# Kernel optimization log

Hardware: AMD Instinct MI355X
Metric: run time of the kernel (lower is better)

The kernel has to match this reference:

```python
import jax, jax.numpy as jnp
import numpy as np

EPS = 1e-6
STRIDES = (8, 16, 32)
IOU_THR = 0.5
GAMMA = 2.0
ALPHA = 1.0


def _ciou(b1, b2):
    # b1, b2: [..., 4] xywh boxes (broadcastable). Returns CIOU [...].
    b1xy, b1wh = b1[..., :2], b1[..., 2:]
    b2xy, b2wh = b2[..., :2], b2[..., 2:]
    b1lt, b1rb = b1xy - b1wh * 0.5, b1xy + b1wh * 0.5
    b2lt, b2rb = b2xy - b2wh * 0.5, b2xy + b2wh * 0.5
    lo1, hi1 = jnp.minimum(b1lt, b1rb), jnp.maximum(b1lt, b1rb)
    lo2, hi2 = jnp.minimum(b2lt, b2rb), jnp.maximum(b2lt, b2rb)
    area1 = (hi1[..., 0] - lo1[..., 0]) * (hi1[..., 1] - lo1[..., 1])
    area2 = (hi2[..., 0] - lo2[..., 0]) * (hi2[..., 1] - lo2[..., 1])
    iwh = jnp.clip(jnp.minimum(hi1, hi2) - jnp.maximum(lo1, lo2), 0.0, None)
    inter = iwh[..., 0] * iwh[..., 1]
    union = area1 + area2 - inter
    ious = inter / jnp.maximum(union, EPS)
    # smallest enclosing box diagonal
    owh = jnp.maximum(hi1, hi2) - jnp.minimum(lo1, lo2)
    c2 = jnp.maximum(owh[..., 0] ** 2 + owh[..., 1] ** 2, EPS)
    rho2 = jnp.sum((b1xy - b2xy) ** 2, axis=-1)
    u = rho2 / c2
    v = (4.0 / (np.pi ** 2)) * (
        jnp.arctan(b2wh[..., 0] / jnp.maximum(b2wh[..., 1], EPS))
        - jnp.arctan(b1wh[..., 0] / jnp.maximum(b1wh[..., 1], EPS))
    ) ** 2
    alpha = v / jnp.maximum(1.0 - ious + v, EPS)
    return ious - (u + alpha * v)


def _bce_logits(x, t):
    # stable BCEWithLogits, reduction='none'
    return jnp.logaddexp(0.0, x) - x * t


def _focal(x, t):
    return _bce_logits(x, t) * ALPHA * jnp.abs(t - jax.nn.sigmoid(x)) ** GAMMA


def _layer_loss(p, p_d, label, bboxes, stride):
    bs, grid = p.shape[0], p.shape[1]
    img_size = float(stride * grid)
    p_conf = p[..., 4:5]
    p_cls = p[..., 5:]
    p_d_xywh = p_d[..., :4]
    label_xywh = label[..., :4]
    obj = label[..., 4:5]
    mix = label[..., 5:6]
    label_cls = label[..., 6:]

    ciou = _ciou(p_d_xywh, label_xywh)[..., None]
    scale = 2.0 - label_xywh[..., 2:3] * label_xywh[..., 3:4] / (img_size ** 2)
    loss_ciou = obj * scale * (1.0 - ciou) * mix

    # pairwise CIOU between every pred box and up to 150 GT boxes: [bs,g,g,A,150]
    iou = _ciou(p_d_xywh[..., None, :], bboxes[:, None, None, None, :, :])
    iou_max = jnp.max(iou, axis=-1, keepdims=True)
    noobj = (1.0 - obj) * (iou_max < IOU_THR).astype(p.dtype)

    focal = _focal(p_conf, obj)
    loss_conf = (obj * focal + noobj * focal) * mix
    loss_cls = obj * _bce_logits(p_cls, label_cls) * mix

    l_ciou = jnp.sum(loss_ciou) / bs
    l_conf = jnp.sum(loss_conf) / bs
    l_cls = jnp.sum(loss_cls) / bs
    return l_ciou, l_conf, l_cls


def setup_inputs() -> dict:
    key = jax.random.key(0)
    B, A, NC, IMG = 4, 3, 20, 608
    grids = [76, 38, 19]
    inp = {}
    for i, g in enumerate(grids):
        k = jax.random.fold_in(key, i)
        ks = jax.random.split(k, 10)
        inp[f"p{i}"] = jax.random.normal(ks[0], (B, g, g, A, 5 + NC), jnp.float32)
        # decoded predictions: positive xywh in image coords + raw conf/cls
        xy = jax.random.uniform(ks[1], (B, g, g, A, 2)) * IMG
        wh = jax.random.uniform(ks[2], (B, g, g, A, 2)) * 120.0 + 2.0
        cc = jax.random.normal(ks[3], (B, g, g, A, 1 + NC))
        inp[f"p_d{i}"] = jnp.concatenate([xy, wh, cc], -1)
        # labels: xywh, obj (binary), mix (1.0), cls (binary)
        lxy = jax.random.uniform(ks[4], (B, g, g, A, 2)) * IMG
        lwh = jax.random.uniform(ks[5], (B, g, g, A, 2)) * 120.0 + 2.0
        obj = (jax.random.uniform(ks[6], (B, g, g, A, 1)) < 0.05).astype(jnp.float32)
        mix = jnp.ones((B, g, g, A, 1), jnp.float32)
        cls = (jax.random.uniform(ks[7], (B, g, g, A, NC)) < 0.5).astype(jnp.float32)
        inp[f"label{i}"] = jnp.concatenate([lxy, lwh, obj, mix, cls], -1)
        bxy = jax.random.uniform(ks[8], (B, 150, 2)) * IMG
        bwh = jax.random.uniform(ks[9], (B, 150, 2)) * 120.0 + 2.0
        inp[f"bboxes{i}"] = jnp.concatenate([bxy, bwh], -1)
    return inp


def reference(p0, p1, p2, p_d0, p_d1, p_d2, label0, label1, label2,
              bboxes0, bboxes1, bboxes2):
    ls_c, ls_conf, ls_cls = _layer_loss(p0, p_d0, label0, bboxes0, STRIDES[0])
    lm_c, lm_conf, lm_cls = _layer_loss(p1, p_d1, label1, bboxes1, STRIDES[1])
    ll_c, ll_conf, ll_cls = _layer_loss(p2, p_d2, label2, bboxes2, STRIDES[2])
    loss_ciou = ls_c + lm_c + ll_c
    loss_conf = ls_conf + lm_conf + ll_conf
    loss_cls = ls_cls + lm_cls + ll_cls
    loss = loss_ciou + loss_conf + loss_cls
    return (loss, loss_ciou, loss_conf, loss_cls)
```

## Files before the change

### kernel.cpp

```cpp
#include <hip/hip_runtime.h>
#include <math.h>

#define EPS   1e-6f
#define K_V   0.4052847345693511f
#define IMG2  369664.0f
#define NBOX  150
#define NBOXP 152
#define NCLS  20

#define BPB_L0 271
#define BPB_L1 68
#define BPB_L2 17
#define NBLK   (4*(BPB_L0+BPB_L1+BPB_L2))

#define NDW_P  1600
#define NDW_LB 1664

__device__ __forceinline__ float fast_rcp(float x) { return __builtin_amdgcn_rcpf(x); }

__device__ __forceinline__ float bce_logits(float x, float t) {
    float e = __expf(-fabsf(x));
    return fmaxf(x, 0.f) + __logf(1.f + e) - x * t;
}

__device__ __forceinline__ float wave_sum(float v) {
#pragma unroll
    for (int off = 32; off > 0; off >>= 1) v += __shfl_down(v, off, 64);
    return v;
}

__device__ __forceinline__ void stage(const float* __restrict__ g, float* s,
                                      size_t g0, size_t tot, int ndw,
                                      int wave, int lane) {
    for (int base = wave * 64; base < ndw; base += 256) {
        if (g0 + base + 64 <= tot) {
            __builtin_amdgcn_global_load_lds(
                (const __attribute__((address_space(1))) void*)(g + base + lane),
                (__attribute__((address_space(3))) void*)(s + base), 4, 0, 0);
        } else {
            int idx = base + lane;
            s[idx] = (g0 + idx < tot) ? g[idx] : 0.f;
        }
    }
}

__global__ __launch_bounds__(256, 6) void yolo_loss_kernel(
    const float* __restrict__ p0,  const float* __restrict__ pd0,
    const float* __restrict__ lb0, const float* __restrict__ bb0,
    const float* __restrict__ p1,  const float* __restrict__ pd1,
    const float* __restrict__ lb1, const float* __restrict__ bb1,
    const float* __restrict__ p2,  const float* __restrict__ pd2,
    const float* __restrict__ lb2, const float* __restrict__ bb2,
    float* __restrict__ ws, float* __restrict__ out)
{
    __shared__ float  s_pd[NDW_P], s_lb[NDW_LB], s_p[NDW_P];
    __shared__ float4 s_box[NBOXP];
    __shared__ float4 s_aux[NBOXP];
    __shared__ float  s_part[4][3];

    const int blk = blockIdx.x;
    const float *p, *pd, *lb, *bb;
    int batch, lblk, apb;
    if (blk < 4*BPB_L0) {
        p = p0; pd = pd0; lb = lb0; bb = bb0;
        batch = blk / BPB_L0; lblk = blk % BPB_L0; apb = 17328;
    } else if (blk < 4*(BPB_L0+BPB_L1)) {
        int r = blk - 4*BPB_L0;
        p = p1; pd = pd1; lb = lb1; bb = bb1;
        batch = r / BPB_L1; lblk = r % BPB_L1; apb = 4332;
    } else {
        int r = blk - 4*(BPB_L0+BPB_L1);
        p = p2; pd = pd2; lb = lb2; bb = bb2;
        batch = r / BPB_L2; lblk = r % BPB_L2; apb = 1083;
    }

    const int tid  = threadIdx.x;
    const int wave = tid >> 6, lane = tid & 63;
    const int navail = min(64, apb - lblk * 64);
    const size_t base0 = (size_t)batch * apb + (size_t)lblk * 64;

    const size_t g0p  = base0 * 25, g0lb = base0 * 26;
    const size_t totp = (size_t)apb * 100;
    const size_t totlb = (size_t)apb * 104;
    stage(pd + g0p,  s_pd, g0p,  totp,  NDW_P,  wave, lane);
    stage(lb + g0lb, s_lb, g0lb, totlb, NDW_LB, wave, lane);
    stage(p + g0p,   s_p,  g0p,  totp,  NDW_P,  wave, lane);

    if (tid < NBOXP) {
        float4 bxy = make_float4(3.0e30f, 3.0e30f, 0.f, 1.f);
        if (tid < NBOX) bxy = ((const float4*)bb)[batch * NBOX + tid];
        float hw = bxy.z * 0.5f, hh = bxy.w * 0.5f;
        float ltx = bxy.x - hw, lty = bxy.y - hh, rbx = bxy.x + hw, rby = bxy.y + hh;
        float lox = fminf(ltx, rbx), hix = fmaxf(ltx, rbx);
        float loy = fminf(lty, rby), hiy = fmaxf(lty, rby);
        s_box[tid] = make_float4(lox, loy, hix, hiy);
        s_aux[tid] = make_float4((hix - lox) * (hiy - loy), bxy.x, bxy.y,
                                 atanf(bxy.z / fmaxf(bxy.w, EPS)));
    }
    __syncthreads();

    const int q = lane >> 4, s = lane & 15;
    const int row = wave * 16 + s;
    const bool active = (row < navail);

    const float b1x = s_pd[row*25 + 0], b1y = s_pd[row*25 + 1];
    const float b1w = s_pd[row*25 + 2], b1h = s_pd[row*25 + 3];
    const float obj = s_lb[row*26 + 4], mix = s_lb[row*26 + 5];
    const float pconf = s_p[row*25 + 4];

    const float hw = b1w * 0.5f, hh = b1h * 0.5f;
    const float l1x = b1x - hw, l1y = b1y - hh;
    const float r1x = b1x + hw, r1y = b1y + hh;
    const float lo1x = fminf(l1x, r1x), hi1x = fmaxf(l1x, r1x);
    const float lo1y = fminf(l1y, r1y), hi1y = fmaxf(l1y, r1y);
    const float area1 = (hi1x - lo1x) * (hi1y - lo1y);

    const int j0 = q * 38;
    unsigned long long mask = 0ull;
    if (active && obj == 0.f) {
#pragma unroll 4
        for (int k = 0; k < 38; ++k) {
            float4 b4 = s_box[j0 + k];
            float a2  = s_aux[j0 + k].x;
            float ix0 = fmaxf(lo1x, b4.x), iy0 = fmaxf(lo1y, b4.y);
            float ix1 = fminf(hi1x, b4.z), iy1 = fminf(hi1y, b4.w);
            float iwx = fmaxf(ix1 - ix0, 0.f);
            float iwy = fmaxf(iy1 - iy0, 0.f);
            float inter = iwx * iwy;
            float uni_m = fmaxf(area1 + a2 - inter, EPS);
            float metric = fmaf(-0.999996f, uni_m, inter + inter);
            mask |= (unsigned long long)(metric > 0.f) << k;
        }
    }

    int hit = 0;
    if (mask) {
        const float at1 = atanf(b1w / fmaxf(b1h, EPS));
        unsigned long long m = mask;
        do {
            int k = __ffsll(m) - 1; m &= m - 1;
            float4 b4 = s_box[j0 + k];
            float4 ax = s_aux[j0 + k];
            float ix0 = fmaxf(lo1x, b4.x), iy0 = fmaxf(lo1y, b4.y);
            float ix1 = fminf(hi1x, b4.z), iy1 = fminf(hi1y, b4.w);
            float iwx = fmaxf(ix1 - ix0, 0.f);
            float iwy = fmaxf(iy1 - iy0, 0.f);
            float inter = iwx * iwy;
            float iou = inter * fast_rcp(fmaxf(area1 + ax.x - inter, EPS));
            float owx = fmaxf(hi1x, b4.z) - fminf(lo1x, b4.x);
            float owy = fmaxf(hi1y, b4.w) - fminf(lo1y, b4.y);
            float c2 = fmaxf(owx * owx + owy * owy, EPS);
            float dx = b1x - ax.y, dy = b1y - ax.z;
            float u = (dx * dx + dy * dy) * fast_rcp(c2);
            float dv = ax.w - at1;
            float v = K_V * dv * dv;
            float alpha = v * fast_rcp(fmaxf(1.f - iou + v, EPS));
            float ci = iou - (u + alpha * v);
            hit |= (ci >= 0.5f);
        } while (m);
    }
    hit |= __shfl_xor(hit, 16, 64);
    hit |= __shfl_xor(hit, 32, 64);

    float t_ciou = 0.f, t_conf = 0.f, t_cls = 0.f;
    if (active && obj > 0.f) {
        float cs = 0.f;
#pragma unroll
        for (int c = 0; c < 5; ++c) {
            int cc = q * 5 + c;
            cs += bce_logits(s_p[row*25 + 5 + cc], s_lb[row*26 + 6 + cc]);
        }
        t_cls = cs * mix;
    }
    if (active && q == 0) {
        const float sig = fast_rcp(1.f + __expf(-pconf));
        const float dd = fabsf(obj - sig);
        const float focal = bce_logits(pconf, obj) * (dd * dd);
        float gate;
        if (obj > 0.f) {
            const float at1 = atanf(b1w / fmaxf(b1h, EPS));
            const float lx = s_lb[row*26 + 0], ly = s_lb[row*26 + 1];
            const float lw = s_lb[row*26 + 2], lh = s_lb[row*26 + 3];
            const float hlw = lw * 0.5f, hlh = lh * 0.5f;
            const float l2x = lx - hlw, l2y = ly - hlh;
            const float r2x = lx + hlw, r2y = ly + hlh;
            const float lo2x = fminf(l2x, r2x), hi2x = fmaxf(l2x, r2x);
            const float lo2y = fminf(l2y, r2y), hi2y = fmaxf(l2y, r2y);
            const float area2 = (hi2x - lo2x) * (hi2y - lo2y);
            float iwx = fmaxf(fminf(hi1x, hi2x) - fmaxf(lo1x, lo2x), 0.f);
            float iwy = fmaxf(fminf(hi1y, hi2y) - fmaxf(lo1y, lo2y), 0.f);
            float inter = iwx * iwy;
            float iou = inter * fast_rcp(fmaxf(area1 + area2 - inter, EPS));
            float owx = fmaxf(hi1x, hi2x) - fminf(lo1x, lo2x);
            float owy = fmaxf(hi1y, hi2y) - fminf(lo1y, lo2y);
            float c2 = fmaxf(owx * owx + owy * owy, EPS);
            float dx = b1x - lx, dy = b1y - ly;
            float u = (dx * dx + dy * dy) * fast_rcp(c2);
            float at2 = atanf(lw / fmaxf(lh, EPS));
            float dv = at2 - at1;
            float v = K_V * dv * dv;
            float alpha = v * fast_rcp(fmaxf(1.f - iou + v, EPS));
            float ciou = iou - (u + alpha * v);

            float scale = 2.f - lw * lh * (1.f / IMG2);
            t_ciou = scale * (1.f - ciou) * mix;
            gate = 1.f;
        } else {
            gate = hit ? 0.f : 1.f;
        }
        t_conf = gate * focal * mix;
    }

    float r0 = wave_sum(t_ciou);
    float r1 = wave_sum(t_conf);
    float r2 = wave_sum(t_cls);
    if (lane == 0) { s_part[wave][0] = r0; s_part[wave][1] = r1; s_part[wave][2] = r2; }
    __syncthreads();

    if (tid == 0) {
        float c = 0.f, f = 0.f, cl = 0.f;
#pragma unroll
        for (int w = 0; w < 4; ++w) { c += s_part[w][0]; f += s_part[w][1]; cl += s_part[w][2]; }
        const int slot = (blk & 7) * 16;
        atomicAdd(&ws[slot + 0], c);
        atomicAdd(&ws[slot + 1], f);
        atomicAdd(&ws[slot + 2], cl);
        __threadfence();
        unsigned old = atomicAdd((unsigned*)(ws + 128), 1u);
        if (old == NBLK - 1) {
            __threadfence();
            float C = 0.f, F = 0.f, CL = 0.f;
#pragma unroll
            for (int sl = 0; sl < 8; ++sl) {
                C  += atomicAdd(&ws[sl*16 + 0], 0.f);
                F  += atomicAdd(&ws[sl*16 + 1], 0.f);
                CL += atomicAdd(&ws[sl*16 + 2], 0.f);
            }
            const float inv_bs = 0.25f;
            out[0] = (C + F + CL) * inv_bs;
            out[1] = C * inv_bs;
            out[2] = F * inv_bs;
            out[3] = CL * inv_bs;
        }
    }
}

extern "C" void kernel_launch(void* const* d_in, const int* in_sizes, int n_in,
                              void* d_out, int out_size, void* d_ws, size_t ws_size,
                              hipStream_t stream) {
    const float* p0  = (const float*)d_in[0];
    const float* pd0 = (const float*)d_in[1];
    const float* lb0 = (const float*)d_in[2];
    const float* bb0 = (const float*)d_in[3];
    const float* p1  = (const float*)d_in[4];
    const float* pd1 = (const float*)d_in[5];
    const float* lb1 = (const float*)d_in[6];
    const float* bb1 = (const float*)d_in[7];
    const float* p2  = (const float*)d_in[8];
    const float* pd2 = (const float*)d_in[9];
    const float* lb2 = (const float*)d_in[10];
    const float* bb2 = (const float*)d_in[11];

    float* ws = (float*)d_ws;
    hipMemsetAsync(ws, 0, 132 * sizeof(float), stream);

    yolo_loss_kernel<<<NBLK, 256, 0, stream>>>(
        p0, pd0, lb0, bb0, p1, pd1, lb1, bb1, p2, pd2, lb2, bb2,
        ws, (float*)d_out);
}
```

Baseline: 127.4 us.

## Convert to persistent blocks pulling tiles from an atomic work queue

Launches a fixed grid of 1024 blocks that repeatedly grab tile indices from a global atomic counter instead of one block per tile. Each block keeps per-thread loss accumulators across tiles and rebuilds the GT box table in shared memory only when the layer/batch changes. The scan loop now recomputes box area from the box corners rather than reading it from the aux array, and the occupancy hint drops from 6 to 4 blocks per CU. It aims to cut per-block setup and redundant box preprocessing, at the cost of an extra atomic plus a block barrier per tile, and staging that is not overlapped with compute.

```diff
diff --git a/kernel.cpp b/kernel.cpp
--- a/kernel.cpp
+++ b/kernel.cpp
@@ -8,10 +8,11 @@
 #define NBOXP 152
 #define NCLS  20
 
-#define BPB_L0 271
-#define BPB_L1 68
-#define BPB_L2 17
-#define NBLK   (4*(BPB_L0+BPB_L1+BPB_L2))
+#define TPB_L0 271
+#define TPB_L1 68
+#define TPB_L2 17
+#define NT     (4*(TPB_L0+TPB_L1+TPB_L2))
+#define GRID   1024
 
 #define NDW_P  1600
 #define NDW_LB 1664
@@ -44,7 +45,7 @@
     }
 }
 
-__global__ __launch_bounds__(256, 6) void yolo_loss_kernel(
+__global__ __launch_bounds__(256, 4) void yolo_loss_kernel(
     const float* __restrict__ p0,  const float* __restrict__ pd0,
     const float* __restrict__ lb0, const float* __restrict__ bb0,
     const float* __restrict__ p1,  const float* __restrict__ pd1,
@@ -57,163 +58,175 @@
     __shared__ float4 s_box[NBOXP];
     __shared__ float4 s_aux[NBOXP];
     __shared__ float  s_part[4][3];
-
-    const int blk = blockIdx.x;
-    const float *p, *pd, *lb, *bb;
-    int batch, lblk, apb;
-    if (blk < 4*BPB_L0) {
-        p = p0; pd = pd0; lb = lb0; bb = bb0;
-        batch = blk / BPB_L0; lblk = blk % BPB_L0; apb = 17328;
-    } else if (blk < 4*(BPB_L0+BPB_L1)) {
-        int r = blk - 4*BPB_L0;
-        p = p1; pd = pd1; lb = lb1; bb = bb1;
-        batch = r / BPB_L1; lblk = r % BPB_L1; apb = 4332;
-    } else {
-        int r = blk - 4*(BPB_L0+BPB_L1);
-        p = p2; pd = pd2; lb = lb2; bb = bb2;
-        batch = r / BPB_L2; lblk = r % BPB_L2; apb = 1083;
-    }
+    __shared__ int    s_t;
 
     const int tid  = threadIdx.x;
     const int wave = tid >> 6, lane = tid & 63;
-    const int navail = min(64, apb - lblk * 64);
-    const size_t base0 = (size_t)batch * apb + (size_t)lblk * 64;
-
-    const size_t g0p  = base0 * 25, g0lb = base0 * 26;
-    const size_t totp = (size_t)apb * 100;
-    const size_t totlb = (size_t)apb * 104;
-    stage(pd + g0p,  s_pd, g0p,  totp,  NDW_P,  wave, lane);
-    stage(lb + g0lb, s_lb, g0lb, totlb, NDW_LB, wave, lane);
-    stage(p + g0p,   s_p,  g0p,  totp,  NDW_P,  wave, lane);
-
-    if (tid < NBOXP) {
-        float4 bxy = make_float4(3.0e30f, 3.0e30f, 0.f, 1.f);
-        if (tid < NBOX) bxy = ((const float4*)bb)[batch * NBOX + tid];
-        float hw = bxy.z * 0.5f, hh = bxy.w * 0.5f;
-        float ltx = bxy.x - hw, lty = bxy.y - hh, rbx = bxy.x + hw, rby = bxy.y + hh;
-        float lox = fminf(ltx, rbx), hix = fmaxf(ltx, rbx);
-        float loy = fminf(lty, rby), hiy = fmaxf(lty, rby);
-        s_box[tid] = make_float4(lox, loy, hix, hiy);
-        s_aux[tid] = make_float4((hix - lox) * (hiy - loy), bxy.x, bxy.y,
-                                 atanf(bxy.z / fmaxf(bxy.w, EPS)));
-    }
-    __syncthreads();
-
     const int q = lane >> 4, s = lane & 15;
     const int row = wave * 16 + s;
-    const bool active = (row < navail);
-
-    const float b1x = s_pd[row*25 + 0], b1y = s_pd[row*25 + 1];
-    const float b1w = s_pd[row*25 + 2], b1h = s_pd[row*25 + 3];
-    const float obj = s_lb[row*26 + 4], mix = s_lb[row*26 + 5];
-    const float pconf = s_p[row*25 + 4];
-
-    const float hw = b1w * 0.5f, hh = b1h * 0.5f;
-    const float l1x = b1x - hw, l1y = b1y - hh;
-    const float r1x = b1x + hw, r1y = b1y + hh;
-    const float lo1x = fminf(l1x, r1x), hi1x = fmaxf(l1x, r1x);
-    const float lo1y = fminf(l1y, r1y), hi1y = fmaxf(l1y, r1y);
-    const float area1 = (hi1x - lo1x) * (hi1y - lo1y);
-
-    const int j0 = q * 38;
-    unsigned long long mask = 0ull;
-    if (active && obj == 0.f) {
+
+    float acc0 = 0.f, acc1 = 0.f, acc2 = 0.f;
+    int cur = -1;
+
+    for (;;) {
+        if (tid == 0) s_t = (int)atomicAdd((unsigned*)(ws + 129), 1u);
+        __syncthreads();
+        const int t = s_t;
+        if (t >= NT) break;
+
+        const float *p, *pd, *lb, *bb;
+        int batch, lblk, apb, layer;
+        if (t < 4*TPB_L0) {
+            layer = 0; p = p0; pd = pd0; lb = lb0; bb = bb0;
+            batch = t / TPB_L0; lblk = t % TPB_L0; apb = 17328;
+        } else if (t < 4*(TPB_L0+TPB_L1)) {
+            int r = t - 4*TPB_L0;
+            layer = 1; p = p1; pd = pd1; lb = lb1; bb = bb1;
+            batch = r / TPB_L1; lblk = r % TPB_L1; apb = 4332;
+        } else {
+            int r = t - 4*(TPB_L0+TPB_L1);
+            layer = 2; p = p2; pd = pd2; lb = lb2; bb = bb2;
+            batch = r / TPB_L2; lblk = r % TPB_L2; apb = 1083;
+        }
+        const int key = layer * 4 + batch;
+        const int navail = min(64, apb - lblk * 64);
+        const size_t base0 = (size_t)batch * apb + (size_t)lblk * 64;
+
+        const size_t g0p = base0 * 25, g0lb = base0 * 26;
+        const size_t totp = (size_t)apb * 100, totlb = (size_t)apb * 104;
+        stage(pd + g0p,  s_pd, g0p,  totp,  NDW_P,  wave, lane);
+        stage(lb + g0lb, s_lb, g0lb, totlb, NDW_LB, wave, lane);
+        stage(p + g0p,   s_p,  g0p,  totp,  NDW_P,  wave, lane);
+
+        if (key != cur) {
+            cur = key;
+            if (tid < NBOXP) {
+                float4 bxy = make_float4(3.0e30f, 3.0e30f, 0.f, 1.f);
+                if (tid < NBOX) bxy = ((const float4*)bb)[batch * NBOX + tid];
+                float hw = bxy.z * 0.5f, hh = bxy.w * 0.5f;
+                float ltx = bxy.x - hw, lty = bxy.y - hh;
+                float rbx = bxy.x + hw, rby = bxy.y + hh;
+                float lox = fminf(ltx, rbx), hix = fmaxf(ltx, rbx);
+                float loy = fminf(lty, rby), hiy = fmaxf(lty, rby);
+                s_box[tid] = make_float4(lox, loy, hix, hiy);
+                s_aux[tid] = make_float4((hix - lox) * (hiy - loy), bxy.x, bxy.y,
+                                         atanf(bxy.z / fmaxf(bxy.w, EPS)));
+            }
+        }
+        __syncthreads();
+
+        const bool active = (row < navail);
+
+        const float b1x = s_pd[row*25 + 0], b1y = s_pd[row*25 + 1];
+        const float b1w = s_pd[row*25 + 2], b1h = s_pd[row*25 + 3];
+        const float obj = s_lb[row*26 + 4], mix = s_lb[row*26 + 5];
+        const float pconf = s_p[row*25 + 4];
+
+        const float hw = b1w * 0.5f, hh = b1h * 0.5f;
+        const float l1x = b1x - hw, l1y = b1y - hh;
+        const float r1x = b1x + hw, r1y = b1y + hh;
+        const float lo1x = fminf(l1x, r1x), hi1x = fmaxf(l1x, r1x);
+        const float lo1y = fminf(l1y, r1y), hi1y = fmaxf(l1y, r1y);
+        const float area1 = (hi1x - lo1x) * (hi1y - lo1y);
+
+        const int j0 = q * 38;
+        unsigned long long mask = 0ull;
+        if (active && obj == 0.f) {
 #pragma unroll 4
-        for (int k = 0; k < 38; ++k) {
-            float4 b4 = s_box[j0 + k];
-            float a2  = s_aux[j0 + k].x;
-            float ix0 = fmaxf(lo1x, b4.x), iy0 = fmaxf(lo1y, b4.y);
-            float ix1 = fminf(hi1x, b4.z), iy1 = fminf(hi1y, b4.w);
-            float iwx = fmaxf(ix1 - ix0, 0.f);
-            float iwy = fmaxf(iy1 - iy0, 0.f);
-            float inter = iwx * iwy;
-            float uni_m = fmaxf(area1 + a2 - inter, EPS);
-            float metric = fmaf(-0.999996f, uni_m, inter + inter);
-            mask |= (unsigned long long)(metric > 0.f) << k;
+            for (int k = 0; k < 38; ++k) {
+                float4 b4 = s_box[j0 + k];
+                float a2  = (b4.z - b4.x) * (b4.w - b4.y);
+                float ix0 = fmaxf(lo1x, b4.x), iy0 = fmaxf(lo1y, b4.y);
+                float ix1 = fminf(hi1x, b4.z), iy1 = fminf(hi1y, b4.w);
+                float iwx = fmaxf(ix1 - ix0, 0.f);
+                float iwy = fmaxf(iy1 - iy0, 0.f);
+                float inter = iwx * iwy;
+                float uni_m = fmaxf(area1 + a2 - inter, EPS);
+                float metric = fmaf(-0.999996f, uni_m, inter + inter);
+                mask |= (unsigned long long)(metric > 0.f) << k;
+            }
+        }
+
+        int hit = 0;
+        if (mask) {
+            const float at1 = atanf(b1w / fmaxf(b1h, EPS));
+            unsigned long long m = mask;
+            do {
+                int k = __ffsll(m) - 1; m &= m - 1;
+                float4 b4 = s_box[j0 + k];
+                float4 ax = s_aux[j0 + k];
+                float ix0 = fmaxf(lo1x, b4.x), iy0 = fmaxf(lo1y, b4.y);
+                float ix1 = fminf(hi1x, b4.z), iy1 = fminf(hi1y, b4.w);
+                float iwx = fmaxf(ix1 - ix0, 0.f);
+                float iwy = fmaxf(iy1 - iy0, 0.f);
+                float inter = iwx * iwy;
+                float iou = inter * fast_rcp(fmaxf(area1 + ax.x - inter, EPS));
+                float owx = fmaxf(hi1x, b4.z) - fminf(lo1x, b4.x);
+                float owy = fmaxf(hi1y, b4.w) - fminf(lo1y, b4.y);
+                float c2 = fmaxf(owx * owx + owy * owy, EPS);
+                float dx = b1x - ax.y, dy = b1y - ax.z;
+                float u = (dx * dx + dy * dy) * fast_rcp(c2);
+                float dv = ax.w - at1;
+                float v = K_V * dv * dv;
+                float alpha = v * fast_rcp(fmaxf(1.f - iou + v, EPS));
+                float ci = iou - (u + alpha * v);
+                hit |= (ci >= 0.5f);
+            } while (m);
+        }
+        hit |= __shfl_xor(hit, 16, 64);
+        hit |= __shfl_xor(hit, 32, 64);
+
+        if (active && obj > 0.f) {
+            float cs = 0.f;
+#pragma unroll
+            for (int c = 0; c < 5; ++c) {
+                int cc = q * 5 + c;
+                cs += bce_logits(s_p[row*25 + 5 + cc], s_lb[row*26 + 6 + cc]);
+            }
+            acc2 += cs * mix;
+        }
+        if (active && q == 0) {
+            const float sig = fast_rcp(1.f + __expf(-pconf));
+            const float dd = fabsf(obj - sig);
+            const float focal = bce_logits(pconf, obj) * (dd * dd);
+            float gate;
+            if (obj > 0.f) {
+                const float at1 = atanf(b1w / fmaxf(b1h, EPS));
+                const float lx = s_lb[row*26 + 0], ly = s_lb[row*26 + 1];
+                const float lw = s_lb[row*26 + 2], lh = s_lb[row*26 + 3];
+                const float hlw = lw * 0.5f, hlh = lh * 0.5f;
+                const float l2x = lx - hlw, l2y = ly - hlh;
+                const float r2x = lx + hlw, r2y = ly + hlh;
+                const float lo2x = fminf(l2x, r2x), hi2x = fmaxf(l2x, r2x);
+                const float lo2y = fminf(l2y, r2y), hi2y = fmaxf(l2y, r2y);
+                const float area2 = (hi2x - lo2x) * (hi2y - lo2y);
+                float iwx = fmaxf(fminf(hi1x, hi2x) - fmaxf(lo1x, lo2x), 0.f);
+                float iwy = fmaxf(fminf(hi1y, hi2y) - fmaxf(lo1y, lo2y), 0.f);
+                float inter = iwx * iwy;
+                float iou = inter * fast_rcp(fmaxf(area1 + area2 - inter, EPS));
+                float owx = fmaxf(hi1x, hi2x) - fminf(lo1x, lo2x);
+                float owy = fmaxf(hi1y, hi2y) - fminf(lo1y, lo2y);
+                float c2 = fmaxf(owx * owx + owy * owy, EPS);
+                float dx = b1x - lx, dy = b1y - ly;
+                float u = (dx * dx + dy * dy) * fast_rcp(c2);
+                float at2 = atanf(lw / fmaxf(lh, EPS));
+                float dv = at2 - at1;
+                float v = K_V * dv * dv;
+                float alpha = v * fast_rcp(fmaxf(1.f - iou + v, EPS));
+                float ciou = iou - (u + alpha * v);
+                float scale = 2.f - lw * lh * (1.f / IMG2);
+                acc0 += scale * (1.f - ciou) * mix;
+                gate = 1.f;
+            } else {
+                gate = hit ? 0.f : 1.f;
+            }
+            acc1 += gate * focal * mix;
         }
     }
 
-    int hit = 0;
-    if (mask) {
-        const float at1 = atanf(b1w / fmaxf(b1h, EPS));
-        unsigned long long m = mask;
-        do {
-            int k = __ffsll(m) - 1; m &= m - 1;
-            float4 b4 = s_box[j0 + k];
-            float4 ax = s_aux[j0 + k];
-            float ix0 = fmaxf(lo1x, b4.x), iy0 = fmaxf(lo1y, b4.y);
-            float ix1 = fminf(hi1x, b4.z), iy1 = fminf(hi1y, b4.w);
-            float iwx = fmaxf(ix1 - ix0, 0.f);
-            float iwy = fmaxf(iy1 - iy0, 0.f);
-            float inter = iwx * iwy;
-            float iou = inter * fast_rcp(fmaxf(area1 + ax.x - inter, EPS));
-            float owx = fmaxf(hi1x, b4.z) - fminf(lo1x, b4.x);
-            float owy = fmaxf(hi1y, b4.w) - fminf(lo1y, b4.y);
-            float c2 = fmaxf(owx * owx + owy * owy, EPS);
-            float dx = b1x - ax.y, dy = b1y - ax.z;
-            float u = (dx * dx + dy * dy) * fast_rcp(c2);
-            float dv = ax.w - at1;
-            float v = K_V * dv * dv;
-            float alpha = v * fast_rcp(fmaxf(1.f - iou + v, EPS));
-            float ci = iou - (u + alpha * v);
-            hit |= (ci >= 0.5f);
-        } while (m);
-    }
-    hit |= __shfl_xor(hit, 16, 64);
-    hit |= __shfl_xor(hit, 32, 64);
-
-    float t_ciou = 0.f, t_conf = 0.f, t_cls = 0.f;
-    if (active && obj > 0.f) {
-        float cs = 0.f;
-#pragma unroll
-        for (int c = 0; c < 5; ++c) {
-            int cc = q * 5 + c;
-            cs += bce_logits(s_p[row*25 + 5 + cc], s_lb[row*26 + 6 + cc]);
-        }
-        t_cls = cs * mix;
-    }
-    if (active && q == 0) {
-        const float sig = fast_rcp(1.f + __expf(-pconf));
-        const float dd = fabsf(obj - sig);
-        const float focal = bce_logits(pconf, obj) * (dd * dd);
-        float gate;
-        if (obj > 0.f) {
-            const float at1 = atanf(b1w / fmaxf(b1h, EPS));
-            const float lx = s_lb[row*26 + 0], ly = s_lb[row*26 + 1];
-            const float lw = s_lb[row*26 + 2], lh = s_lb[row*26 + 3];
-            const float hlw = lw * 0.5f, hlh = lh * 0.5f;
-            const float l2x = lx - hlw, l2y = ly - hlh;
-            const float r2x = lx + hlw, r2y = ly + hlh;
-            const float lo2x = fminf(l2x, r2x), hi2x = fmaxf(l2x, r2x);
-            const float lo2y = fminf(l2y, r2y), hi2y = fmaxf(l2y, r2y);
-            const float area2 = (hi2x - lo2x) * (hi2y - lo2y);
-            float iwx = fmaxf(fminf(hi1x, hi2x) - fmaxf(lo1x, lo2x), 0.f);
-            float iwy = fmaxf(fminf(hi1y, hi2y) - fmaxf(lo1y, lo2y), 0.f);
-            float inter = iwx * iwy;
-            float iou = inter * fast_rcp(fmaxf(area1 + area2 - inter, EPS));
-            float owx = fmaxf(hi1x, hi2x) - fminf(lo1x, lo2x);
-            float owy = fmaxf(hi1y, hi2y) - fminf(lo1y, lo2y);
-            float c2 = fmaxf(owx * owx + owy * owy, EPS);
-            float dx = b1x - lx, dy = b1y - ly;
-            float u = (dx * dx + dy * dy) * fast_rcp(c2);
-            float at2 = atanf(lw / fmaxf(lh, EPS));
-            float dv = at2 - at1;
-            float v = K_V * dv * dv;
-            float alpha = v * fast_rcp(fmaxf(1.f - iou + v, EPS));
-            float ciou = iou - (u + alpha * v);
-
-            float scale = 2.f - lw * lh * (1.f / IMG2);
-            t_ciou = scale * (1.f - ciou) * mix;
-            gate = 1.f;
-        } else {
-            gate = hit ? 0.f : 1.f;
-        }
-        t_conf = gate * focal * mix;
-    }
-
-    float r0 = wave_sum(t_ciou);
-    float r1 = wave_sum(t_conf);
-    float r2 = wave_sum(t_cls);
+    float r0 = wave_sum(acc0);
+    float r1 = wave_sum(acc1);
+    float r2 = wave_sum(acc2);
     if (lane == 0) { s_part[wave][0] = r0; s_part[wave][1] = r1; s_part[wave][2] = r2; }
     __syncthreads();
 
@@ -221,13 +234,13 @@
         float c = 0.f, f = 0.f, cl = 0.f;
 #pragma unroll
         for (int w = 0; w < 4; ++w) { c += s_part[w][0]; f += s_part[w][1]; cl += s_part[w][2]; }
-        const int slot = (blk & 7) * 16;
+        const int slot = (blockIdx.x & 7) * 16;
         atomicAdd(&ws[slot + 0], c);
         atomicAdd(&ws[slot + 1], f);
         atomicAdd(&ws[slot + 2], cl);
         __threadfence();
         unsigned old = atomicAdd((unsigned*)(ws + 128), 1u);
-        if (old == NBLK - 1) {
+        if (old == GRID - 1) {
             __threadfence();
             float C = 0.f, F = 0.f, CL = 0.f;
 #pragma unroll
@@ -264,7 +277,7 @@
     float* ws = (float*)d_ws;
     hipMemsetAsync(ws, 0, 132 * sizeof(float), stream);
 
-    yolo_loss_kernel<<<NBLK, 256, 0, stream>>>(
+    yolo_loss_kernel<<<GRID, 256, 0, stream>>>(
         p0, pd0, lb0, bb0, p1, pd1, lb1, bb1, p2, pd2, lb2, bb2,
         ws, (float*)d_out);
 }
```

After: 138.1 us. +8.4%, slower.
